# Kernel optimization log

Measured on AMD Instinct MI355X. Metric: run time of the kernel, lower is better.

The kernel has to match this reference:

```python
import jax, jax.numpy as jnp
import numpy as np

N, T, C1, C2, H = 32, 64, 128, 256, 512
LN2 = float(np.log(2.0))
EPS = 1e-8  # torch CosineSimilarity default eps


def setup_inputs() -> dict:
    key = jax.random.key(0)
    ks = jax.random.split(key, 16)
    g = lambda k, shape, fan: jax.random.normal(k, shape, jnp.float32) / np.sqrt(fan)
    inp = {
        "h0": jax.random.normal(ks[0], (N, H), jnp.float32),
        "c0": jax.random.normal(ks[1], (N, C1, C2), jnp.float32),
        "c_x": jax.random.normal(ks[2], (N, T, C1, C2), jnp.float32),
        # linear_k / linear_b / linear_e / linear_v (torch Linear: y = x W^T + b)
        "Wk": g(ks[3], (C2, H), H), "bk": jnp.zeros((C2,), jnp.float32),
        "Wb": g(ks[4], (1, H), H),  "bb": jnp.zeros((1,), jnp.float32),
        "We": g(ks[5], (C2, H), H), "be": jnp.zeros((C2,), jnp.float32),
        "Wv": g(ks[6], (C2, H), H), "bv": jnp.zeros((C2,), jnp.float32),
        # GRUCell(C2 -> H): packed [r|z|n] gates
        "W_ih": g(ks[7], (3 * H, C2), C2), "b_ih": jnp.zeros((3 * H,), jnp.float32),
        "W_hh": g(ks[8], (3 * H, H), H),   "b_hh": jnp.zeros((3 * H,), jnp.float32),
    }
    return inp


def _gru_cell(x, h, W_ih, b_ih, W_hh, b_hh):
    gi = x @ W_ih.T + b_ih  # (N, 3H)
    gh = h @ W_hh.T + b_hh
    i_r, i_z, i_n = jnp.split(gi, 3, axis=-1)
    h_r, h_z, h_n = jnp.split(gh, 3, axis=-1)
    r = jax.nn.sigmoid(i_r + h_r)
    z = jax.nn.sigmoid(i_z + h_z)
    n = jnp.tanh(i_n + r * h_n)
    return (1.0 - z) * n + z * h


def _ntm_step(p, h_prev, c_prev, cx):
    # h_prev: (N,H), c_prev/cx: (N,C1,C2)
    k = h_prev @ p["Wk"].T + p["bk"]              # (N,C2) key
    beta_pre = h_prev @ p["Wb"].T + p["bb"]       # (N,1)
    bpos = jnp.maximum(beta_pre, 0.0)
    bneg = jnp.minimum(beta_pre, 0.0)
    beta = jnp.log1p(jnp.exp(bneg)) + bpos + jnp.log1p(jnp.exp(-bpos)) + (1.0 - LN2)
    # cosine similarity along C2 between each memory row and the key
    num = jnp.einsum("nic,nc->ni", cx, k)         # (N,C1)
    cn = jnp.linalg.norm(cx, axis=2)              # (N,C1)
    kn = jnp.linalg.norm(k, axis=1, keepdims=True)  # (N,1)
    s = num / jnp.maximum(cn * kn, EPS)
    w = jax.nn.softmax(s * beta, axis=1)          # (N,C1) addressing weights
    r = jnp.einsum("ni,nic->nc", w, cx)           # (N,C2) read vector
    h = _gru_cell(r, h_prev, p["W_ih"], p["b_ih"], p["W_hh"], p["b_hh"])
    e = jax.nn.sigmoid(h @ p["We"].T + p["be"])   # (N,C2) erase
    v = h @ p["Wv"].T + p["bv"]                   # (N,C2) add
    wc = w[:, :, None]                            # (N,C1,1)
    c_new = c_prev * (1.0 - wc * e[:, None, :]) + wc * v[:, None, :]
    return h, c_new


def _forward(h0, c0, c_x, Wk, bk, Wb, bb, We, be, Wv, bv, W_ih, b_ih, W_hh, b_hh):
    p = dict(Wk=Wk, bk=bk, Wb=Wb, bb=bb, We=We, be=be, Wv=Wv, bv=bv,
             W_ih=W_ih, b_ih=b_ih, W_hh=W_hh, b_hh=b_hh)

    def step(carry, cx_t):
        h, c = carry
        h2, c2 = _ntm_step(p, h, c, cx_t)
        return (h2, c2), (h2, c2)

    _, (hs, cs) = jax.lax.scan(step, (h0, c0), jnp.swapaxes(c_x, 0, 1))
    # (T,N,...) -> (N,T,...)
    return jnp.swapaxes(hs, 0, 1), jnp.swapaxes(cs, 0, 1)


def reference(h0, c0, c_x, Wk, bk, Wb, bb, We, be, Wv, bv, W_ih, b_ih, W_hh, b_hh):
    return _forward(h0, c0, c_x, Wk, bk, Wb, bb, We, be, Wv, bv, W_ih, b_ih, W_hh, b_hh)
```

## Files before the change

### kernel.cpp

```cpp
#include <hip/hip_runtime.h>
#include <math.h>


#define NBAT 32
#define TSTEPS 64
#define C1D 128
#define C2D 256
#define HD 512
#define NBLK 128
#define LN2F 0.6931471805599453f

typedef float f32x4 __attribute__((ext_vector_type(4)));

static __device__ __forceinline__ float dot4f(float4 a, float4 b) {
  return a.x * b.x + a.y * b.y + a.z * b.z + a.w * b.w;
}
static __device__ __forceinline__ float sigm(float x) { return 1.0f / (1.0f + __expf(-x)); }

static __device__ __forceinline__ float aload(const float* p) {
  return __hip_atomic_load(p, __ATOMIC_RELAXED, __HIP_MEMORY_SCOPE_AGENT);
}
static __device__ __forceinline__ void astore(float* p, float v) {
  __hip_atomic_store(p, v, __ATOMIC_RELAXED, __HIP_MEMORY_SCOPE_AGENT);
}
static __device__ __forceinline__ float2 aload2(const float* p) {
  unsigned long long u = __hip_atomic_load((const unsigned long long*)p,
                                           __ATOMIC_RELAXED, __HIP_MEMORY_SCOPE_AGENT);
  union { unsigned long long u; float2 f; } c;
  c.u = u;
  return c.f;
}
static __device__ __forceinline__ void astore2(float* p, float a, float b) {
  union { float f[2]; unsigned long long u; } c;
  c.f[0] = a; c.f[1] = b;
  __hip_atomic_store((unsigned long long*)p, c.u, __ATOMIC_RELAXED, __HIP_MEMORY_SCOPE_AGENT);
}
static __device__ __forceinline__ float4 aload4(const float* p) {
  const float2 lo = aload2(p), hi = aload2(p + 2);
  return make_float4(lo.x, lo.y, hi.x, hi.y);
}

__global__ void __launch_bounds__(256) ntm_chain(
    const float* __restrict__ h0, const float* __restrict__ c_x,
    const float* __restrict__ Wk, const float* __restrict__ bk,
    const float* __restrict__ Wb, const float* __restrict__ bb,
    const float* __restrict__ We, const float* __restrict__ be,
    const float* __restrict__ Wv, const float* __restrict__ bv,
    const float* __restrict__ Wih, const float* __restrict__ bih,
    const float* __restrict__ Whh, const float* __restrict__ bhh,
    float* __restrict__ hs_out, float* __restrict__ wsf, unsigned* __restrict__ flags)
{
  const int tid = threadIdx.x;
  const int bid = blockIdx.x;

  float* hb0   = wsf;
  float* hb1   = hb0 + NBAT * HD;
  float* kbuf  = hb1 + NBAT * HD;
  float* betab = kbuf + NBAT * C2D;
  float* rbuf  = betab + 64;
  float* wbuf  = rbuf + NBAT * C2D;
  float* earr  = wbuf + NBAT * TSTEPS * C1D;
  float* varr  = earr + NBAT * TSTEPS * C2D;

  __shared__ float s_k[C2D];
  __shared__ float s_sc[C1D];
  __shared__ float s_w[C1D];
  __shared__ float s_misc[8];
  __shared__ float s_r[NBAT * 264];
  __shared__ float s_wih[12 * 260];
  __shared__ float s_whh[12 * 516];
  __shared__ float s_wk[2 * 516];
  __shared__ float s_wev[8 * 516];
  __shared__ float s_wb[HD];

  const int j0 = bid * 4;
  const int kch = bid * 2;
  const int evch = (bid - 32) * 4;

  for (int idx = tid; idx < 12 * C2D; idx += 256) {
    const int row = idx >> 8, c = idx & (C2D - 1);
    const int f = row / 3, g = row % 3;
    s_wih[row * 260 + c] = Wih[(g * HD + j0 + f) * C2D + c];
  }
  for (int idx = tid; idx < 12 * HD; idx += 256) {
    const int row = idx >> 9, c = idx & (HD - 1);
    const int f = row / 3, g = row % 3;
    s_whh[row * 516 + c] = Whh[(g * HD + j0 + f) * HD + c];
  }
  for (int idx = tid; idx < 2 * HD; idx += 256) {
    const int row = idx >> 9, c = idx & (HD - 1);
    s_wk[row * 516 + c] = Wk[(kch + row) * HD + c];
  }
  if (bid >= 32 && bid < 96) {
    for (int idx = tid; idx < 8 * HD; idx += 256) {
      const int row = idx >> 9, c = idx & (HD - 1);
      const float* __restrict__ src = (row < 4) ? We : Wv;
      s_wev[row * 516 + c] = src[(evch + (row & 3)) * HD + c];
    }
  }
  for (int idx = tid; idx < HD; idx += 256) s_wb[idx] = Wb[idx];
  __syncthreads();

  unsigned gen = 0;
  auto gridbar = [&]() {
    ++gen;
    asm volatile("s_waitcnt vmcnt(0) lgkmcnt(0)" ::: "memory");
    __syncthreads();
    if (tid == 0)
      __hip_atomic_store(flags + bid * 32, gen, __ATOMIC_RELAXED, __HIP_MEMORY_SCOPE_AGENT);
    if (tid < 64) {
      const unsigned* f0 = flags + (2 * tid) * 32;
      const unsigned* f1 = flags + (2 * tid + 1) * 32;
      while (true) {
        const unsigned a = __hip_atomic_load(f0, __ATOMIC_RELAXED, __HIP_MEMORY_SCOPE_AGENT);
        const unsigned b = __hip_atomic_load(f1, __ATOMIC_RELAXED, __HIP_MEMORY_SCOPE_AGENT);
        if (__all(a >= gen && b >= gen)) break;
        __builtin_amdgcn_s_sleep(2);
      }
    }
    __syncthreads();
  };

  auto proj_k = [&](const float* __restrict__ hsrc) {
    const int n = tid >> 3, s = tid & 7;
    const float* hp = hsrc + n * HD;
    float k0 = 0, k1 = 0, bp = 0;
#pragma unroll
    for (int x = 0; x < 16; ++x) {
      const int cix = s * 64 + ((4 * x + 8 * s) & 63);
      const float4 hv = aload4(hp + cix);
      k0 += dot4f(hv, *(const float4*)(s_wk + cix));
      k1 += dot4f(hv, *(const float4*)(s_wk + 516 + cix));
      if (bid == 0) bp += dot4f(hv, *(const float4*)(s_wb + cix));
    }
#pragma unroll
    for (int m = 1; m < 8; m <<= 1) { k0 += __shfl_xor(k0, m); k1 += __shfl_xor(k1, m); }
    if (bid == 0) {
#pragma unroll
      for (int m = 1; m < 8; m <<= 1) bp += __shfl_xor(bp, m);
    }
    if (s == 0) {
      astore2(kbuf + n * C2D + kch, k0 + bk[kch], k1 + bk[kch + 1]);
      if (bid == 0) {
        const float xb = bp + bb[0];
        const float bpos = fmaxf(xb, 0.f), bneg = fminf(xb, 0.f);
        astore(betab + n, log1pf(__expf(bneg)) + bpos + log1pf(__expf(-bpos)) + (1.0f - LN2F));
      }
    }
  };

  auto phase_ev = [&](const float* __restrict__ hsrc, int te) {
    const int n = tid >> 3, s = tid & 7;
    const float* hp = hsrc + n * HD;
    float e[4] = {0, 0, 0, 0}, v[4] = {0, 0, 0, 0};
#pragma unroll
    for (int x = 0; x < 16; ++x) {
      const int cix = s * 64 + ((4 * x + 8 * s) & 63);
      const float4 hv = aload4(hp + cix);
#pragma unroll
      for (int f = 0; f < 4; ++f) {
        e[f] += dot4f(hv, *(const float4*)(s_wev + f * 516 + cix));
        v[f] += dot4f(hv, *(const float4*)(s_wev + (4 + f) * 516 + cix));
      }
    }
#pragma unroll
    for (int m = 1; m < 8; m <<= 1) {
#pragma unroll
      for (int f = 0; f < 4; ++f) { e[f] += __shfl_xor(e[f], m); v[f] += __shfl_xor(v[f], m); }
    }
    if (s == 0) {
      *(float4*)(earr + (size_t)(n * TSTEPS + te) * C2D + evch) =
          make_float4(sigm(e[0] + be[evch]), sigm(e[1] + be[evch + 1]),
                      sigm(e[2] + be[evch + 2]), sigm(e[3] + be[evch + 3]));
      *(float4*)(varr + (size_t)(n * TSTEPS + te) * C2D + evch) =
          make_float4(v[0] + bv[evch], v[1] + bv[evch + 1],
                      v[2] + bv[evch + 2], v[3] + bv[evch + 3]);
    }
  };

  auto phase_attn = [&](int t) {
    const int n = bid;
    const float* cxt = c_x + (size_t)(n * TSTEPS + t) * C1D * C2D;
    if (tid < 64) {
      const float4 kv = aload4(kbuf + n * C2D + tid * 4);
      *(float4*)(s_k + tid * 4) = kv;
      float sq = kv.x * kv.x + kv.y * kv.y + kv.z * kv.z + kv.w * kv.w;
#pragma unroll
      for (int m = 1; m < 64; m <<= 1) sq += __shfl_xor(sq, m);
      if (tid == 0) s_misc[0] = sqrtf(sq);
    } else if (tid == 64) {
      s_misc[1] = aload(betab + n);
    }
    __syncthreads();
    {
      const int row = tid >> 1, half = tid & 1;
      const float* xp = cxt + row * C2D + half * 128;
      const float* kp = s_k + half * 128;
      float np = 0, cp = 0;
#pragma unroll
      for (int x = 0; x < 32; ++x) {
        const float4 xv = *(const float4*)(xp + x * 4);
        np += dot4f(xv, *(const float4*)(kp + x * 4));
        cp += dot4f(xv, xv);
      }
      np += __shfl_xor(np, 1);
      cp += __shfl_xor(cp, 1);
      if (half == 0)
        s_sc[row] = s_misc[1] * np / fmaxf(sqrtf(cp) * s_misc[0], 1e-8f);
    }
    __syncthreads();
    if (tid < 64) {
      const float a = s_sc[tid], b = s_sc[tid + 64];
      float mx = fmaxf(a, b);
#pragma unroll
      for (int m = 1; m < 64; m <<= 1) mx = fmaxf(mx, __shfl_xor(mx, m));
      const float p0 = __expf(a - mx), p1 = __expf(b - mx);
      float L = p0 + p1;
#pragma unroll
      for (int m = 1; m < 64; m <<= 1) L += __shfl_xor(L, m);
      const float iL = 1.f / L;
      const float w0 = p0 * iL, w1 = p1 * iL;
      s_w[tid] = w0;
      s_w[tid + 64] = w1;
      wbuf[(size_t)(n * TSTEPS + t) * C1D + tid] = w0;
      wbuf[(size_t)(n * TSTEPS + t) * C1D + tid + 64] = w1;
    }
    __syncthreads();
    {
      const int c = tid;
      float acc = 0.f;
#pragma unroll 8
      for (int i = 0; i < C1D; ++i) acc += s_w[i] * cxt[i * C2D + c];
      astore(rbuf + n * C2D + c, acc);
    }
  };

  auto phase_gru = [&](const float* __restrict__ hsrc, float* __restrict__ hdst, int t) {
#pragma unroll
    for (int idx = tid; idx < 2048; idx += 256) {
      const int n2 = idx >> 6, c4 = (idx & 63) * 4;
      const float4 rv = aload4(rbuf + n2 * C2D + c4);
      *(float4*)(s_r + n2 * 264 + c4) = rv;
    }
    __syncthreads();
    const int n = tid >> 3, s = tid & 7;
    float aR[4] = {0, 0, 0, 0}, aZ[4] = {0, 0, 0, 0};
    float aNi[4] = {0, 0, 0, 0}, aNh[4] = {0, 0, 0, 0};
    const float* rb = s_r + n * 264 + s * 32;
#pragma unroll
    for (int x = 0; x < 8; ++x) {
      const int o = (4 * x + 4 * s) & 31;
      const float4 rv = *(const float4*)(rb + o);
      const int cix = s * 32 + o;
#pragma unroll
      for (int f = 0; f < 4; ++f) {
        aR[f]  += dot4f(rv, *(const float4*)(s_wih + (f * 3 + 0) * 260 + cix));
        aZ[f]  += dot4f(rv, *(const float4*)(s_wih + (f * 3 + 1) * 260 + cix));
        aNi[f] += dot4f(rv, *(const float4*)(s_wih + (f * 3 + 2) * 260 + cix));
      }
    }
    const float* hb = hsrc + n * HD;
#pragma unroll
    for (int x = 0; x < 16; ++x) {
      const int cix = s * 64 + ((4 * x + 8 * s) & 63);
      const float4 hv = aload4(hb + cix);
#pragma unroll
      for (int f = 0; f < 4; ++f) {
        aR[f]  += dot4f(hv, *(const float4*)(s_whh + (f * 3 + 0) * 516 + cix));
        aZ[f]  += dot4f(hv, *(const float4*)(s_whh + (f * 3 + 1) * 516 + cix));
        aNh[f] += dot4f(hv, *(const float4*)(s_whh + (f * 3 + 2) * 516 + cix));
      }
    }
#pragma unroll
    for (int m = 1; m < 8; m <<= 1) {
#pragma unroll
      for (int f = 0; f < 4; ++f) {
        aR[f] += __shfl_xor(aR[f], m);
        aZ[f] += __shfl_xor(aZ[f], m);
        aNi[f] += __shfl_xor(aNi[f], m);
        aNh[f] += __shfl_xor(aNh[f], m);
      }
    }
    if (s == 0) {
      const float4 hp4 = aload4(hsrc + n * HD + j0);
      const float hpv[4] = {hp4.x, hp4.y, hp4.z, hp4.w};
      float hn[4];
#pragma unroll
      for (int f = 0; f < 4; ++f) {
        const int j = j0 + f;
        const float rg = sigm(aR[f] + bih[j] + bhh[j]);
        const float z = sigm(aZ[f] + bih[HD + j] + bhh[HD + j]);
        const float ng = tanhf(aNi[f] + bih[2 * HD + j] + rg * (aNh[f] + bhh[2 * HD + j]));
        hn[f] = (1.f - z) * ng + z * hpv[f];
      }
      astore2(hdst + n * HD + j0, hn[0], hn[1]);
      astore2(hdst + n * HD + j0 + 2, hn[2], hn[3]);
      *(float4*)(hs_out + (size_t)(n * TSTEPS + t) * HD + j0) =
          make_float4(hn[0], hn[1], hn[2], hn[3]);
    }
  };

  proj_k(h0);
  gridbar();
  for (int t = 0; t < TSTEPS; ++t) {
    const float* hsrc = (t == 0) ? h0 : ((t & 1) ? hb0 : hb1);
    float* hdst = (t & 1) ? hb1 : hb0;
    if (bid < 32) phase_attn(t);
    else if (bid < 96 && t > 0) phase_ev(hsrc, t - 1);
    gridbar();
    phase_gru(hsrc, hdst, t);
    gridbar();
    if (t < TSTEPS - 1) {
      proj_k(hdst);
      gridbar();
    }
  }
  if (bid >= 32 && bid < 96) phase_ev(hb1, TSTEPS - 1);
}

__global__ void __launch_bounds__(256) ntm_cscan(
    const float* __restrict__ c0, const float* __restrict__ wsf,
    float* __restrict__ out)
{
  const float* wbuf = wsf + 2 * NBAT * HD + NBAT * C2D + 64 + NBAT * C2D;
  const float* earr = wbuf + NBAT * TSTEPS * C1D;
  const float* varr = earr + NBAT * TSTEPS * C2D;
  float* cs_out = out + NBAT * TSTEPS * HD;

  const int tid = threadIdx.x;
  const int lane = tid & 63, wid = tid >> 6;
  const int n = blockIdx.x >> 3, g = blockIdx.x & 7;
  const int i0 = g * 16 + wid * 4;

  f32x4 c[4];
#pragma unroll
  for (int r = 0; r < 4; ++r)
    c[r] = *(const f32x4*)(c0 + ((size_t)(n * C1D + i0 + r)) * C2D + lane * 4);

  const float* ep = earr + (size_t)n * TSTEPS * C2D + lane * 4;
  const float* vp = varr + (size_t)n * TSTEPS * C2D + lane * 4;
  const float* wp = wbuf + (size_t)n * TSTEPS * C1D + i0;

  f32x4 e_nxt = *(const f32x4*)(ep);
  f32x4 v_nxt = *(const f32x4*)(vp);
  for (int t = 0; t < TSTEPS; ++t) {
    const f32x4 e4 = e_nxt, v4 = v_nxt;
    if (t + 1 < TSTEPS) {
      e_nxt = *(const f32x4*)(ep + (t + 1) * C2D);
      v_nxt = *(const f32x4*)(vp + (t + 1) * C2D);
    }
#pragma unroll
    for (int r = 0; r < 4; ++r) {
      const float wr = wp[t * C1D + r];
      c[r] = c[r] * (1.f - wr * e4) + wr * v4;
      __builtin_nontemporal_store(
          c[r], (f32x4*)(cs_out + ((size_t)((n * TSTEPS + t) * C1D + i0 + r)) * C2D + lane * 4));
    }
  }
}

extern "C" void kernel_launch(void* const* d_in, const int* in_sizes, int n_in,
                              void* d_out, int out_size, void* d_ws, size_t ws_size,
                              hipStream_t stream) {
  const float* h0 = (const float*)d_in[0];
  const float* c0 = (const float*)d_in[1];
  const float* c_x = (const float*)d_in[2];
  const float* Wk = (const float*)d_in[3];
  const float* bk = (const float*)d_in[4];
  const float* Wb = (const float*)d_in[5];
  const float* bb = (const float*)d_in[6];
  const float* We = (const float*)d_in[7];
  const float* be = (const float*)d_in[8];
  const float* Wv = (const float*)d_in[9];
  const float* bv = (const float*)d_in[10];
  const float* Wih = (const float*)d_in[11];
  const float* bih = (const float*)d_in[12];
  const float* Whh = (const float*)d_in[13];
  const float* bhh = (const float*)d_in[14];

  unsigned* flags = (unsigned*)d_ws;
  float* wsf = (float*)((char*)d_ws + 16384);

  (void)hipMemsetAsync(d_ws, 0, 16384, stream);
  ntm_chain<<<dim3(NBLK), dim3(256), 0, stream>>>(h0, c_x, Wk, bk, Wb, bb, We, be, Wv, bv,
                                                  Wih, bih, Whh, bhh, (float*)d_out, wsf, flags);
  ntm_cscan<<<dim3(256), dim3(256), 0, stream>>>(c0, wsf, (float*)d_out);
}
```

Baseline: 3.062 ms.

## Split attention across all blocks with flash-style combine and point-to-point flags

Spreads the per-batch attention phase over four blocks per batch, each handling 32 memory rows from a shared-memory tile prefetched one step ahead. Partial max, sum and read vectors are merged by a combine block using online-softmax rescaling. The generic grid barriers are replaced by per-phase flag counters, so blocks wait only on the producers they depend on, and the erase/add projection moves off the critical path. The cost is extra global traffic for the partials, a second hop through the combine block, and more complex synchronisation.

```diff
diff --git a/kernel.cpp b/kernel.cpp
--- a/kernel.cpp
+++ b/kernel.cpp
@@ -9,6 +9,7 @@
 #define HD 512
 #define NBLK 128
 #define LN2F 0.6931471805599453f
+#define PSTRIDE 296
 
 typedef float f32x4 __attribute__((ext_vector_type(4)));
 
@@ -39,6 +40,18 @@
   const float2 lo = aload2(p), hi = aload2(p + 2);
   return make_float4(lo.x, lo.y, hi.x, hi.y);
 }
+static __device__ __forceinline__ unsigned aloadu(const unsigned* p) {
+  return __hip_atomic_load(p, __ATOMIC_RELAXED, __HIP_MEMORY_SCOPE_AGENT);
+}
+static __device__ __forceinline__ void astoreu(unsigned* p, unsigned v) {
+  __hip_atomic_store(p, v, __ATOMIC_RELAXED, __HIP_MEMORY_SCOPE_AGENT);
+}
+static __device__ __forceinline__ void spinu(const unsigned* p, unsigned tgt) {
+  while (aloadu(p) < tgt) __builtin_amdgcn_s_sleep(4);
+}
+
+#define BLOCK_FENCE() \
+  do { asm volatile("s_waitcnt vmcnt(0) lgkmcnt(0)" ::: "memory"); __syncthreads(); } while (0)
 
 __global__ void __launch_bounds__(256) ntm_chain(
     const float* __restrict__ h0, const float* __restrict__ c_x,
@@ -52,27 +65,33 @@
 {
   const int tid = threadIdx.x;
   const int bid = blockIdx.x;
+  const int lane = tid & 63;
+  const int wid = tid >> 6;
 
   float* hb0   = wsf;
   float* hb1   = hb0 + NBAT * HD;
   float* kbuf  = hb1 + NBAT * HD;
   float* betab = kbuf + NBAT * C2D;
   float* rbuf  = betab + 64;
-  float* wbuf  = rbuf + NBAT * C2D;
+  float* part  = rbuf + NBAT * C2D;
+  float* wbuf  = part + NBAT * 4 * PSTRIDE;
   float* earr  = wbuf + NBAT * TSTEPS * C1D;
   float* varr  = earr + NBAT * TSTEPS * C2D;
 
-  __shared__ float s_k[C2D];
-  __shared__ float s_sc[C1D];
-  __shared__ float s_w[C1D];
-  __shared__ float s_misc[8];
+  __shared__ float s_tile[32 * C2D];
   __shared__ float s_r[NBAT * 264];
   __shared__ float s_wih[12 * 260];
   __shared__ float s_whh[12 * 516];
   __shared__ float s_wk[2 * 516];
   __shared__ float s_wev[8 * 516];
   __shared__ float s_wb[HD];
-
+  __shared__ float s_k[C2D];
+  __shared__ float s_sc[32];
+  __shared__ float s_p[32];
+  __shared__ float s_ml[8];
+  __shared__ float s_misc[8];
+
+  const int n_att = bid >> 2, q_att = bid & 3;
   const int j0 = bid * 4;
   const int kch = bid * 2;
   const int evch = (bid - 32) * 4;
@@ -99,26 +118,16 @@
     }
   }
   for (int idx = tid; idx < HD; idx += 256) s_wb[idx] = Wb[idx];
-  __syncthreads();
-
-  unsigned gen = 0;
-  auto gridbar = [&]() {
-    ++gen;
-    asm volatile("s_waitcnt vmcnt(0) lgkmcnt(0)" ::: "memory");
-    __syncthreads();
-    if (tid == 0)
-      __hip_atomic_store(flags + bid * 32, gen, __ATOMIC_RELAXED, __HIP_MEMORY_SCOPE_AGENT);
-    if (tid < 64) {
-      const unsigned* f0 = flags + (2 * tid) * 32;
-      const unsigned* f1 = flags + (2 * tid + 1) * 32;
-      while (true) {
-        const unsigned a = __hip_atomic_load(f0, __ATOMIC_RELAXED, __HIP_MEMORY_SCOPE_AGENT);
-        const unsigned b = __hip_atomic_load(f1, __ATOMIC_RELAXED, __HIP_MEMORY_SCOPE_AGENT);
-        if (__all(a >= gen && b >= gen)) break;
-        __builtin_amdgcn_s_sleep(2);
-      }
-    }
-    __syncthreads();
+
+  float4 pf[8];
+  auto prefetch_issue = [&](int t) {
+    const float* src = c_x + ((size_t)((n_att * TSTEPS + t) * C1D + q_att * 32)) * C2D + lane * 4;
+#pragma unroll
+    for (int k = 0; k < 8; ++k) pf[k] = *(const float4*)(src + (wid * 8 + k) * C2D);
+  };
+  auto prefetch_commit = [&]() {
+#pragma unroll
+    for (int k = 0; k < 8; ++k) *(float4*)(s_tile + (wid * 8 + k) * C2D + lane * 4) = pf[k];
   };
 
   auto proj_k = [&](const float* __restrict__ hsrc) {
@@ -179,60 +188,88 @@
   };
 
   auto phase_attn = [&](int t) {
-    const int n = bid;
-    const float* cxt = c_x + (size_t)(n * TSTEPS + t) * C1D * C2D;
     if (tid < 64) {
-      const float4 kv = aload4(kbuf + n * C2D + tid * 4);
+      const float4 kv = aload4(kbuf + n_att * C2D + tid * 4);
       *(float4*)(s_k + tid * 4) = kv;
       float sq = kv.x * kv.x + kv.y * kv.y + kv.z * kv.z + kv.w * kv.w;
 #pragma unroll
       for (int m = 1; m < 64; m <<= 1) sq += __shfl_xor(sq, m);
       if (tid == 0) s_misc[0] = sqrtf(sq);
     } else if (tid == 64) {
-      s_misc[1] = aload(betab + n);
+      s_misc[1] = aload(betab + n_att);
     }
     __syncthreads();
     {
-      const int row = tid >> 1, half = tid & 1;
-      const float* xp = cxt + row * C2D + half * 128;
-      const float* kp = s_k + half * 128;
+      const int row = tid >> 3, s8 = tid & 7;
+      const float* xp = s_tile + row * C2D + s8 * 32;
+      const float* kp = s_k + s8 * 32;
       float np = 0, cp = 0;
 #pragma unroll
-      for (int x = 0; x < 32; ++x) {
+      for (int x = 0; x < 8; ++x) {
         const float4 xv = *(const float4*)(xp + x * 4);
         np += dot4f(xv, *(const float4*)(kp + x * 4));
         cp += dot4f(xv, xv);
       }
-      np += __shfl_xor(np, 1);
-      cp += __shfl_xor(cp, 1);
-      if (half == 0)
-        s_sc[row] = s_misc[1] * np / fmaxf(sqrtf(cp) * s_misc[0], 1e-8f);
-    }
-    __syncthreads();
-    if (tid < 64) {
-      const float a = s_sc[tid], b = s_sc[tid + 64];
-      float mx = fmaxf(a, b);
-#pragma unroll
-      for (int m = 1; m < 64; m <<= 1) mx = fmaxf(mx, __shfl_xor(mx, m));
-      const float p0 = __expf(a - mx), p1 = __expf(b - mx);
-      float L = p0 + p1;
-#pragma unroll
-      for (int m = 1; m < 64; m <<= 1) L += __shfl_xor(L, m);
-      const float iL = 1.f / L;
-      const float w0 = p0 * iL, w1 = p1 * iL;
-      s_w[tid] = w0;
-      s_w[tid + 64] = w1;
-      wbuf[(size_t)(n * TSTEPS + t) * C1D + tid] = w0;
-      wbuf[(size_t)(n * TSTEPS + t) * C1D + tid + 64] = w1;
+      np += __shfl_xor(np, 1); cp += __shfl_xor(cp, 1);
+      np += __shfl_xor(np, 2); cp += __shfl_xor(cp, 2);
+      np += __shfl_xor(np, 4); cp += __shfl_xor(cp, 4);
+      if (s8 == 0) s_sc[row] = s_misc[1] * np / fmaxf(sqrtf(cp) * s_misc[0], 1e-8f);
+    }
+    __syncthreads();
+    float* pp = part + (size_t)(n_att * 4 + q_att) * PSTRIDE;
+    if (tid < 32) {
+      const float s = s_sc[tid];
+      float mq = s;
+#pragma unroll
+      for (int m = 1; m < 32; m <<= 1) mq = fmaxf(mq, __shfl_xor(mq, m));
+      const float p = __expf(s - mq);
+      s_p[tid] = p;
+      float lq = p;
+#pragma unroll
+      for (int m = 1; m < 32; m <<= 1) lq += __shfl_xor(lq, m);
+      if (tid == 0) astore2(pp, mq, lq);
+      astore(pp + 258 + tid, s);
     }
     __syncthreads();
     {
       const int c = tid;
       float acc = 0.f;
 #pragma unroll 8
-      for (int i = 0; i < C1D; ++i) acc += s_w[i] * cxt[i * C2D + c];
-      astore(rbuf + n * C2D + c, acc);
-    }
+      for (int i = 0; i < 32; ++i) acc += s_p[i] * s_tile[i * C2D + c];
+      astore(pp + 2 + c, acc);
+    }
+    BLOCK_FENCE();
+    if (tid == 0) astoreu(flags + (128 + bid) * 32, (unsigned)(t + 1));
+  };
+
+  auto phase_combine = [&](int t) {
+    const int n = bid >> 2;
+    if (tid < 3) spinu(flags + (128 + bid + 1 + tid) * 32, (unsigned)(t + 1));
+    __syncthreads();
+    if (tid < 4) {
+      const float2 ml = aload2(part + (size_t)(n * 4 + tid) * PSTRIDE);
+      s_ml[2 * tid] = ml.x; s_ml[2 * tid + 1] = ml.y;
+    }
+    __syncthreads();
+    const float M = fmaxf(fmaxf(s_ml[0], s_ml[2]), fmaxf(s_ml[4], s_ml[6]));
+    const float sc0 = __expf(s_ml[0] - M), sc1 = __expf(s_ml[2] - M);
+    const float sc2 = __expf(s_ml[4] - M), sc3 = __expf(s_ml[6] - M);
+    const float invL = 1.f / (s_ml[1] * sc0 + s_ml[3] * sc1 + s_ml[5] * sc2 + s_ml[7] * sc3);
+    if (tid < 128) {
+      const int q = tid >> 5, i = tid & 31;
+      const float s = aload(part + (size_t)(n * 4 + q) * PSTRIDE + 258 + i);
+      wbuf[((size_t)n * TSTEPS + t) * C1D + tid] = __expf(s - M) * invL;
+    }
+    {
+      const int c = tid;
+      const float r = (sc0 * aload(part + (size_t)(n * 4 + 0) * PSTRIDE + 2 + c) +
+                       sc1 * aload(part + (size_t)(n * 4 + 1) * PSTRIDE + 2 + c) +
+                       sc2 * aload(part + (size_t)(n * 4 + 2) * PSTRIDE + 2 + c) +
+                       sc3 * aload(part + (size_t)(n * 4 + 3) * PSTRIDE + 2 + c)) * invL;
+      astore(rbuf + n * C2D + c, r);
+    }
+    BLOCK_FENCE();
+    if (tid == 0) astoreu(flags + (256 + n) * 32, (unsigned)(t + 1));
   };
 
   auto phase_gru = [&](const float* __restrict__ hsrc, float* __restrict__ hdst, int t) {
@@ -298,31 +335,55 @@
       *(float4*)(hs_out + (size_t)(n * TSTEPS + t) * HD + j0) =
           make_float4(hn[0], hn[1], hn[2], hn[3]);
     }
-  };
-
+    BLOCK_FENCE();
+    if (tid == 0) astoreu(flags + (288 + bid) * 32, (unsigned)(t + 1));
+  };
+
+  if (tid < 64) {
+    const int base = bid * 128 + tid * 2;
+    astore2(hb1 + base, h0[base], h0[base + 1]);
+  }
+  prefetch_issue(0);
+  __syncthreads();
+  prefetch_commit();
   proj_k(h0);
-  gridbar();
+  BLOCK_FENCE();
+  if (tid == 0) astoreu(flags + bid * 32, 1u);
+
   for (int t = 0; t < TSTEPS; ++t) {
-    const float* hsrc = (t == 0) ? h0 : ((t & 1) ? hb0 : hb1);
+    const float* hsrc = (t & 1) ? hb0 : hb1;
     float* hdst = (t & 1) ? hb1 : hb0;
-    if (bid < 32) phase_attn(t);
-    else if (bid < 96 && t > 0) phase_ev(hsrc, t - 1);
-    gridbar();
+    if (tid < 64) {
+      spinu(flags + (2 * tid) * 32, (unsigned)(t + 1));
+      spinu(flags + (2 * tid + 1) * 32, (unsigned)(t + 1));
+    }
+    __syncthreads();
+    phase_attn(t);
+    if (t < TSTEPS - 1) prefetch_issue(t + 1);
+    if ((bid & 3) == 0) phase_combine(t);
+    if (t < TSTEPS - 1) prefetch_commit();
+    if (tid < 32) spinu(flags + (256 + tid) * 32, (unsigned)(t + 1));
+    __syncthreads();
     phase_gru(hsrc, hdst, t);
-    gridbar();
+    if (tid < 64) {
+      spinu(flags + (288 + 2 * tid) * 32, (unsigned)(t + 1));
+      spinu(flags + (288 + 2 * tid + 1) * 32, (unsigned)(t + 1));
+    }
+    __syncthreads();
     if (t < TSTEPS - 1) {
       proj_k(hdst);
-      gridbar();
-    }
-  }
-  if (bid >= 32 && bid < 96) phase_ev(hb1, TSTEPS - 1);
+      BLOCK_FENCE();
+      if (tid == 0) astoreu(flags + bid * 32, (unsigned)(t + 2));
+    }
+    if (bid >= 32 && bid < 96) phase_ev(hdst, t);
+  }
 }
 
 __global__ void __launch_bounds__(256) ntm_cscan(
     const float* __restrict__ c0, const float* __restrict__ wsf,
     float* __restrict__ out)
 {
-  const float* wbuf = wsf + 2 * NBAT * HD + NBAT * C2D + 64 + NBAT * C2D;
+  const float* wbuf = wsf + 2 * NBAT * HD + NBAT * C2D + 64 + NBAT * C2D + NBAT * 4 * PSTRIDE;
   const float* earr = wbuf + NBAT * TSTEPS * C1D;
   const float* varr = earr + NBAT * TSTEPS * C2D;
   float* cs_out = out + NBAT * TSTEPS * HD;
@@ -379,9 +440,9 @@
   const float* bhh = (const float*)d_in[14];
 
   unsigned* flags = (unsigned*)d_ws;
-  float* wsf = (float*)((char*)d_ws + 16384);
-
-  (void)hipMemsetAsync(d_ws, 0, 16384, stream);
+  float* wsf = (float*)((char*)d_ws + 65536);
+
+  (void)hipMemsetAsync(d_ws, 0, 65536, stream);
   ntm_chain<<<dim3(NBLK), dim3(256), 0, stream>>>(h0, c_x, Wk, bk, Wb, bb, We, be, Wv, bv,
                                                   Wih, bih, Whh, bhh, (float*)d_out, wsf, flags);
   ntm_cscan<<<dim3(256), dim3(256), 0, stream>>>(c0, wsf, (float*)d_out);
```

Result: faster. 2.791 ms (-8.8%).
